# Kernel tuning notes

Measured on AMD Instinct MI355X. Metric: run time of the kernel, lower is better.

The kernel has to match this reference:

```python
import jax, jax.numpy as jnp
import numpy as np

B, L, D = 2, 2048, 2048
H, HKV, HD = 32, 8, 64
G = H // HKV  # GQA group size


def _rope(t, cos, sin):
    # t: [B, h, L, HD]; cos/sin: [L, HD//2]; pairs are consecutive (view_as_complex)
    tr, ti = t[..., 0::2], t[..., 1::2]
    out_r = tr * cos - ti * sin
    out_i = tr * sin + ti * cos
    return jnp.stack([out_r, out_i], axis=-1).reshape(t.shape)


def setup_inputs() -> dict:
    key = jax.random.key(0)
    ks = jax.random.split(key, 5)
    x = jax.random.normal(ks[0], (B, L, D), dtype=jnp.float32)
    wq = jax.random.normal(ks[1], (D, H * HD), dtype=jnp.float32) * 0.02
    wk = jax.random.normal(ks[2], (D, HKV * HD), dtype=jnp.float32) * 0.02
    wv = jax.random.normal(ks[3], (D, HKV * HD), dtype=jnp.float32) * 0.02
    wo = jax.random.normal(ks[4], (D, D), dtype=jnp.float32) * 0.02
    # RoPE freqs: theta_i = 10000^(-2i/HD), angle[p, i] = p * theta_i
    inv_freq = 1.0 / (10000.0 ** (jnp.arange(0, HD, 2, dtype=jnp.float32) / HD))
    angles = jnp.arange(L, dtype=jnp.float32)[:, None] * inv_freq[None, :]  # [L, HD//2]
    freqs_cos = jnp.cos(angles)
    freqs_sin = jnp.sin(angles)
    # additive causal mask [L, L]
    mask = jnp.where(jnp.tril(jnp.ones((L, L), dtype=bool)), 0.0, -1e9).astype(jnp.float32)
    return {"x": x, "wq": wq, "wk": wk, "wv": wv, "wo": wo,
            "freqs_cos": freqs_cos, "freqs_sin": freqs_sin, "mask": mask}


def reference(x, wq, wk, wv, wo, freqs_cos, freqs_sin, mask):
    b, l, _ = x.shape
    q = (x @ wq).reshape(b, l, H, HD).transpose(0, 2, 1, 3)      # [B, H, L, HD]
    k = (x @ wk).reshape(b, l, HKV, HD).transpose(0, 2, 1, 3)    # [B, HKV, L, HD]
    v = (x @ wv).reshape(b, l, HKV, HD).transpose(0, 2, 1, 3)
    q = _rope(q, freqs_cos, freqs_sin)
    k = _rope(k, freqs_cos, freqs_sin)
    # native GQA broadcast instead of repeat_kv copy (same math)
    qg = q.reshape(b, HKV, G, l, HD)
    scores = jnp.einsum("bhgqd,bhkd->bhgqk", qg, k) / jnp.sqrt(jnp.float32(HD))
    scores = scores + mask  # [B, HKV, G, L, L]
    probs = jax.nn.softmax(scores.astype(jnp.float32), axis=-1).astype(v.dtype)
    out = jnp.einsum("bhgqk,bhkd->bhgqd", probs, v)              # [B, HKV, G, L, HD]
    out = out.reshape(b, H, l, HD).transpose(0, 2, 1, 3).reshape(b, l, H * HD)
    return out @ wo
```

## Files before the change

### kernel.cpp

```cpp
#include <hip/hip_runtime.h>
#include <hip/hip_bf16.h>

#define B_   2
#define L_   2048
#define D_   2048
#define H_   32
#define HKV_ 8
#define HD_  64
#define G_   4
#define M_   4096
#define NF_  3072

typedef __attribute__((ext_vector_type(8))) short bf16x8;
typedef __attribute__((ext_vector_type(4))) float f32x4;

static __device__ __forceinline__ unsigned short f2bf(float f) {
  unsigned int u = __float_as_uint(f);
  unsigned int r = (u + 0x7FFFu + ((u >> 16) & 1u)) >> 16;
  return (unsigned short)r;
}
static __device__ __forceinline__ unsigned short f2bf_hw(float f) {
  __hip_bfloat16 h = __float2bfloat16(f);
  return *(unsigned short*)&h;
}

#define GLD16(g, l) __builtin_amdgcn_global_load_lds(                      \
    (const __attribute__((address_space(1))) void*)(g),                    \
    (__attribute__((address_space(3))) void*)(l), 16, 0, 0)

__global__ void cast_bf16_kernel(const float* __restrict__ in,
                                 unsigned short* __restrict__ out, int n4) {
  int i = blockIdx.x * blockDim.x + threadIdx.x;
  if (i >= n4) return;
  float4 v = ((const float4*)in)[i];
  uint2 r;
  r.x = (unsigned int)f2bf(v.x) | ((unsigned int)f2bf(v.y) << 16);
  r.y = (unsigned int)f2bf(v.z) | ((unsigned int)f2bf(v.w) << 16);
  ((uint2*)out)[i] = r;
}

__global__ void transpose_cast_kernel(const float* __restrict__ src,
                                      unsigned short* __restrict__ dst,
                                      int K, int N) {
  __shared__ float tile[32][33];
  int k0 = blockIdx.y * 32, n0 = blockIdx.x * 32;
  int tx = threadIdx.x, ty = threadIdx.y;
#pragma unroll
  for (int r = 0; r < 4; ++r)
    tile[ty * 4 + r][tx] = src[(size_t)(k0 + ty * 4 + r) * N + n0 + tx];
  __syncthreads();
#pragma unroll
  for (int r = 0; r < 4; ++r)
    dst[(size_t)(n0 + ty * 4 + r) * K + k0 + tx] = f2bf(tile[tx][ty * 4 + r]);
}

__global__ __launch_bounds__(256)
void gemm_bt_kernel(const unsigned short* __restrict__ A,
                    const unsigned short* __restrict__ Bt,
                    float* __restrict__ C, int M, int N, int K) {
  __shared__ unsigned short Al[128 * 32];
  __shared__ unsigned short Bl[128 * 32];
  const int tid = threadIdx.x;
  const int w = tid >> 6;
  const int l = tid & 63;
  const int row0 = blockIdx.y * 128;
  const int col0 = blockIdx.x * 128;
  const int wr = (w >> 1) * 64, wc = (w & 1) * 64;

  f32x4 acc[4][4];
#pragma unroll
  for (int m = 0; m < 4; ++m)
#pragma unroll
    for (int n = 0; n < 4; ++n) acc[m][n] = (f32x4){0.f, 0.f, 0.f, 0.f};

  const int srow = l >> 2;
  const int scol = (l & 3) * 8;
  const int fr = l & 15, fk = (l >> 4) * 8;
  const int nk = K / 32;

  for (int kt = 0; kt < nk; ++kt) {
    const int k0 = kt * 32;
#pragma unroll
    for (int t = 0; t < 2; ++t) {
      const int rr = (w * 2 + t) * 16 + srow;
      GLD16(A + (size_t)(row0 + rr) * K + k0 + scol, &Al[(w * 2 + t) * 512]);
      GLD16(Bt + (size_t)(col0 + rr) * K + k0 + scol, &Bl[(w * 2 + t) * 512]);
    }
    __syncthreads();
    bf16x8 af[4], bfr[4];
#pragma unroll
    for (int m = 0; m < 4; ++m)
      af[m] = *(const bf16x8*)&Al[(wr + m * 16 + fr) * 32 + fk];
#pragma unroll
    for (int n = 0; n < 4; ++n)
      bfr[n] = *(const bf16x8*)&Bl[(wc + n * 16 + fr) * 32 + fk];
#pragma unroll
    for (int m = 0; m < 4; ++m)
#pragma unroll
      for (int n = 0; n < 4; ++n)
        acc[m][n] = __builtin_amdgcn_mfma_f32_16x16x32_bf16(af[m], bfr[n], acc[m][n], 0, 0, 0);
    __syncthreads();
  }

  const int fq = l >> 4;
#pragma unroll
  for (int m = 0; m < 4; ++m)
#pragma unroll
    for (int n = 0; n < 4; ++n)
#pragma unroll
      for (int j = 0; j < 4; ++j) {
        int r = row0 + wr + m * 16 + fq * 4 + j;
        int c = col0 + wc + n * 16 + fr;
        C[(size_t)r * N + c] = acc[m][n][j];
      }
}

__global__ void rope_kernel(const float* __restrict__ src,
                            const float* __restrict__ cosf,
                            const float* __restrict__ sinf,
                            unsigned short* __restrict__ dst, int nh, int col_off,
                            float scale, int total) {
  int idx = blockIdx.x * blockDim.x + threadIdx.x;
  if (idx >= total) return;
  int g = idx & 7;
  int h = (idx >> 3) & (nh - 1);
  int row = idx / (nh << 3);
  int lpos = row & (L_ - 1);
  int b = row >> 11;
  const float* s = src + (size_t)row * NF_ + col_off + h * 64 + g * 8;
  float4 v0 = *(const float4*)s;
  float4 v1 = *(const float4*)(s + 4);
  float4 c4 = *(const float4*)(cosf + lpos * 32 + g * 4);
  float4 s4 = *(const float4*)(sinf + lpos * 32 + g * 4);
  float o0 = (v0.x * c4.x - v0.y * s4.x) * scale;
  float o1 = (v0.x * s4.x + v0.y * c4.x) * scale;
  float o2 = (v0.z * c4.y - v0.w * s4.y) * scale;
  float o3 = (v0.z * s4.y + v0.w * c4.y) * scale;
  float o4 = (v1.x * c4.z - v1.y * s4.z) * scale;
  float o5 = (v1.x * s4.z + v1.y * c4.z) * scale;
  float o6 = (v1.z * c4.w - v1.w * s4.w) * scale;
  float o7 = (v1.z * s4.w + v1.w * c4.w) * scale;
  uint4 r;
  r.x = (unsigned int)f2bf(o0) | ((unsigned int)f2bf(o1) << 16);
  r.y = (unsigned int)f2bf(o2) | ((unsigned int)f2bf(o3) << 16);
  r.z = (unsigned int)f2bf(o4) | ((unsigned int)f2bf(o5) << 16);
  r.w = (unsigned int)f2bf(o6) | ((unsigned int)f2bf(o7) << 16);
  *(uint4*)&dst[(((size_t)(b * nh + h)) * L_ + lpos) * 64 + g * 8] = r;
}

__global__ void cast_vT_kernel(const float* __restrict__ v,
                               unsigned short* __restrict__ vT) {
  __shared__ float tile[32][33];
  int l0 = blockIdx.x * 32, d0 = blockIdx.y * 32;
  int z = blockIdx.z;
  int b = z >> 3, hkv = z & 7;
  int tx = threadIdx.x, ty = threadIdx.y;
  const float* src = v + (size_t)(b * L_) * NF_ + 2560 + hkv * 64;
#pragma unroll
  for (int r = 0; r < 4; ++r)
    tile[ty * 4 + r][tx] = src[(size_t)(l0 + ty * 4 + r) * NF_ + d0 + tx];
  __syncthreads();
  unsigned short* dst = vT + ((size_t)z * 64) * L_;
#pragma unroll
  for (int r = 0; r < 4; ++r)
    dst[(size_t)(d0 + ty * 4 + r) * L_ + l0 + tx] = f2bf(tile[tx][ty * 4 + r]);
}

__global__ __launch_bounds__(256)
void attn_kernel(const unsigned short* __restrict__ Q,
                 const unsigned short* __restrict__ Kt,
                 const unsigned short* __restrict__ Vt,
                 unsigned short* __restrict__ O) {
  __shared__ unsigned short Kl[2][64 * 64];
  __shared__ unsigned short Vl[2][64 * 64];
  __shared__ unsigned short Pl[64 * 64];
  const int tid = threadIdx.x, w = tid >> 6, l = tid & 63;
  const int lin = blockIdx.y * 16 + blockIdx.x;
  const int work = ((lin & 7) << 7) + (lin >> 3);
  const int bh = work >> 4, by = work & 15;
  const int b = bh >> 5, h = bh & 31;
  const int hkv = h >> 2;
  const int q0 = by * 128;
  const int fr = l & 15, hi = l >> 4;
  const int frx = fr & 7;

  const int srow = l >> 3;
  const int scole = ((l & 7) ^ srow) * 8;

  const unsigned short* kbase = Kt + ((size_t)(b * HKV_ + hkv)) * L_ * 64;
  const unsigned short* vbase = Vt + ((size_t)(b * HKV_ + hkv)) * 64 * L_;

  bf16x8 qf[2][2];
#pragma unroll
  for (int s = 0; s < 2; ++s) {
    const unsigned short* qb =
        Q + (((size_t)bh) * L_ + q0 + s * 64 + w * 16 + fr) * 64 + hi * 8;
    qf[s][0] = *(const bf16x8*)(qb);
    qf[s][1] = *(const bf16x8*)(qb + 32);
  }

  float m_i[2][4], l_p[2][4];
  f32x4 oacc[2][4];
#pragma unroll
  for (int s = 0; s < 2; ++s)
#pragma unroll
    for (int j = 0; j < 4; ++j) { m_i[s][j] = -1e30f; l_p[s][j] = 0.f; }
#pragma unroll
  for (int s = 0; s < 2; ++s)
#pragma unroll
    for (int nf = 0; nf < 4; ++nf) oacc[s][nf] = (f32x4){0.f, 0.f, 0.f, 0.f};

  const int nt = 2 * by + 2;

#define ASTAGE(kv0_, buf_) do {                                              \
    _Pragma("unroll")                                                        \
    for (int u_ = 0; u_ < 2; ++u_) {                                         \
      const int c_ = w * 2 + u_;                                             \
      const int rr_ = c_ * 8 + srow;                                         \
      GLD16(kbase + ((size_t)((kv0_) + rr_)) * 64 + scole,                   \
            &Kl[buf_][c_ * 512]);                                            \
      GLD16(vbase + ((size_t)rr_) * L_ + (kv0_) + scole,                     \
            &Vl[buf_][c_ * 512]);                                            \
    }                                                                        \
  } while (0)

  ASTAGE(0, 0);

  for (int t = 0; t < nt; ++t) {
    const int buf = t & 1;
    if (t + 1 < nt) {
      ASTAGE((t + 1) * 64, buf ^ 1);
      asm volatile("s_waitcnt vmcnt(4)" ::: "memory");
    } else {
      asm volatile("s_waitcnt vmcnt(0)" ::: "memory");
    }
    __builtin_amdgcn_s_barrier();

    const int kv0 = t * 64;
#pragma unroll
    for (int s = 0; s < 2; ++s) {
      const int dlim = 2 * by + s;
      if (t > dlim) continue;

      f32x4 sacc[4];
#pragma unroll
      for (int nf = 0; nf < 4; ++nf) sacc[nf] = (f32x4){0.f, 0.f, 0.f, 0.f};
      __builtin_amdgcn_s_setprio(1);
#pragma unroll
      for (int ks = 0; ks < 2; ++ks) {
#pragma unroll
        for (int nf = 0; nf < 4; ++nf) {
          bf16x8 kfrag = *(const bf16x8*)
              &Kl[buf][(nf * 16 + fr) * 64 + (((ks * 4 + hi) ^ frx) * 8)];
          sacc[nf] = __builtin_amdgcn_mfma_f32_16x16x32_bf16(qf[s][ks], kfrag, sacc[nf], 0, 0, 0);
        }
      }
      __builtin_amdgcn_s_setprio(0);

      if (t == dlim) {
        const int rbase = q0 + s * 64 + w * 16 + hi * 4;
#pragma unroll
        for (int nf = 0; nf < 4; ++nf)
#pragma unroll
          for (int j = 0; j < 4; ++j)
            if (kv0 + nf * 16 + fr > rbase + j) sacc[nf][j] = -1e30f;
      }

      float rowmax[4];
#pragma unroll
      for (int j = 0; j < 4; ++j) {
        float mx = fmaxf(fmaxf(sacc[0][j], sacc[1][j]),
                         fmaxf(sacc[2][j], sacc[3][j]));
        mx = fmaxf(mx, __shfl_xor(mx, 1));
        mx = fmaxf(mx, __shfl_xor(mx, 2));
        mx = fmaxf(mx, __shfl_xor(mx, 4));
        mx = fmaxf(mx, __shfl_xor(mx, 8));
        rowmax[j] = mx;
      }

      float g = rowmax[0] - m_i[s][0];
      g = fmaxf(g, rowmax[1] - m_i[s][1]);
      g = fmaxf(g, rowmax[2] - m_i[s][2]);
      g = fmaxf(g, rowmax[3] - m_i[s][3]);
      if (!__all(g <= 8.f)) {
#pragma unroll
        for (int j = 0; j < 4; ++j) {
          float mnew = fmaxf(m_i[s][j], rowmax[j]);
          float cr = exp2f(m_i[s][j] - mnew);
          m_i[s][j] = mnew;
          l_p[s][j] *= cr;
#pragma unroll
          for (int nf = 0; nf < 4; ++nf) oacc[s][nf][j] *= cr;
        }
      }

#pragma unroll
      for (int j = 0; j < 4; ++j) {
        const int prow = w * 16 + hi * 4 + j;
#pragma unroll
        for (int nf = 0; nf < 4; ++nf) {
          float p = exp2f(sacc[nf][j] - m_i[s][j]);
          l_p[s][j] += p;
          Pl[prow * 64 + (((nf * 2 + (fr >> 3)) ^ (prow & 7)) * 8) + frx] =
              f2bf_hw(p);
        }
      }

      __builtin_amdgcn_s_setprio(1);
#pragma unroll
      for (int ks = 0; ks < 2; ++ks) {
        bf16x8 pa = *(const bf16x8*)
            &Pl[(w * 16 + fr) * 64 + (((ks * 4 + hi) ^ frx) * 8)];
#pragma unroll
        for (int nf = 0; nf < 4; ++nf) {
          bf16x8 vfrag = *(const bf16x8*)
              &Vl[buf][(nf * 16 + fr) * 64 + (((ks * 4 + hi) ^ frx) * 8)];
          oacc[s][nf] = __builtin_amdgcn_mfma_f32_16x16x32_bf16(pa, vfrag, oacc[s][nf], 0, 0, 0);
        }
      }
      __builtin_amdgcn_s_setprio(0);
    }
    __builtin_amdgcn_s_barrier();
  }
#undef ASTAGE

#pragma unroll
  for (int s = 0; s < 2; ++s)
#pragma unroll
    for (int j = 0; j < 4; ++j) {
      float lsum = l_p[s][j];
      lsum += __shfl_xor(lsum, 1);
      lsum += __shfl_xor(lsum, 2);
      lsum += __shfl_xor(lsum, 4);
      lsum += __shfl_xor(lsum, 8);
      float inv = 1.0f / lsum;
#pragma unroll
      for (int nf = 0; nf < 4; ++nf) {
        int qrow = q0 + s * 64 + w * 16 + hi * 4 + j;
        int d = nf * 16 + fr;
        O[((size_t)(b * L_ + qrow)) * 2048 + h * 64 + d] =
            f2bf_hw(oacc[s][nf][j] * inv);
      }
    }
}

extern "C" void kernel_launch(void* const* d_in, const int* in_sizes, int n_in,
                              void* d_out, int out_size, void* d_ws, size_t ws_size,
                              hipStream_t stream) {
  (void)in_sizes; (void)n_in; (void)out_size; (void)ws_size;
  const float* x  = (const float*)d_in[0];
  const float* wq = (const float*)d_in[1];
  const float* wk = (const float*)d_in[2];
  const float* wv = (const float*)d_in[3];
  const float* wo = (const float*)d_in[4];
  const float* fc = (const float*)d_in[5];
  const float* fs = (const float*)d_in[6];
  float* out = (float*)d_out;

  char* ws = (char*)d_ws;
  unsigned short* x_b  = (unsigned short*)(ws + 0);
  unsigned short* wT   = (unsigned short*)(ws + 16777216);
  unsigned short* woT  = (unsigned short*)(ws + 29360128);
  float* qkv_f         = (float*)(ws + 37748736);
  unsigned short* at_b = (unsigned short*)(ws + 37748736);
  unsigned short* q_b  = (unsigned short*)(ws + 88080384);
  unsigned short* k_b  = (unsigned short*)(ws + 104857600);
  unsigned short* vT_b = (unsigned short*)(ws + 109051904);

  const float qscale = 0.125f * 1.4426950408889634f;

  dim3 tb(32, 8);
  cast_bf16_kernel<<<8192, 256, 0, stream>>>(x, x_b, M_ * D_ / 4);
  transpose_cast_kernel<<<dim3(64, 64), tb, 0, stream>>>(wq, wT, 2048, 2048);
  transpose_cast_kernel<<<dim3(16, 64), tb, 0, stream>>>(wk, wT + (size_t)2048 * 2048, 2048, 512);
  transpose_cast_kernel<<<dim3(16, 64), tb, 0, stream>>>(wv, wT + (size_t)2560 * 2048, 2048, 512);
  transpose_cast_kernel<<<dim3(64, 64), tb, 0, stream>>>(wo, woT, 2048, 2048);

  gemm_bt_kernel<<<dim3(24, 32), 256, 0, stream>>>(x_b, wT, qkv_f, M_, NF_, 2048);

  rope_kernel<<<4096, 256, 0, stream>>>(qkv_f, fc, fs, q_b, 32, 0, qscale, M_ * 32 * 8);
  rope_kernel<<<1024, 256, 0, stream>>>(qkv_f, fc, fs, k_b, 8, 2048, 1.0f, M_ * 8 * 8);
  cast_vT_kernel<<<dim3(64, 2, 16), tb, 0, stream>>>(qkv_f, vT_b);

  attn_kernel<<<dim3(16, 64), 256, 0, stream>>>(q_b, k_b, vT_b, at_b);

  gemm_bt_kernel<<<dim3(16, 32), 256, 0, stream>>>(at_b, woT, out, M_, 2048, 2048);
}
```

Measured before the change: 449.4 us.

## Balance causal attention by pairing opposite query tiles per block

Each attention block now processes two 64-row query tiles, p and 31-p, in sequence, so every block runs exactly 33 KV tile iterations instead of a count that grows with its query position. This removes the load imbalance of causal attention, where late-row blocks did far more work and set the tail. The per-iteration loop now runs one tile's compute instead of two, so K/V staging is no longer shared across both query halves and the KV prefetch address logic becomes more complex. Separately, the three Q/K/V weight transpose-casts are merged into one launch to save launch overhead.

```diff
diff --git a/kernel.cpp b/kernel.cpp
--- a/kernel.cpp
+++ b/kernel.cpp
@@ -52,6 +52,27 @@
 #pragma unroll
   for (int r = 0; r < 4; ++r)
     dst[(size_t)(n0 + ty * 4 + r) * K + k0 + tx] = f2bf(tile[tx][ty * 4 + r]);
+}
+
+__global__ void transpose_cast_qkv_kernel(const float* __restrict__ wq,
+                                          const float* __restrict__ wk,
+                                          const float* __restrict__ wv,
+                                          unsigned short* __restrict__ dst) {
+  __shared__ float tile[32][33];
+  int n0 = blockIdx.x * 32, k0 = blockIdx.y * 32;
+  const float* src;
+  int ns, N;
+  if (n0 < 2048)      { src = wq; ns = n0;        N = 2048; }
+  else if (n0 < 2560) { src = wk; ns = n0 - 2048; N = 512; }
+  else                { src = wv; ns = n0 - 2560; N = 512; }
+  int tx = threadIdx.x, ty = threadIdx.y;
+#pragma unroll
+  for (int r = 0; r < 4; ++r)
+    tile[ty * 4 + r][tx] = src[(size_t)(k0 + ty * 4 + r) * N + ns + tx];
+  __syncthreads();
+#pragma unroll
+  for (int r = 0; r < 4; ++r)
+    dst[(size_t)(n0 + ty * 4 + r) * 2048 + k0 + tx] = f2bf(tile[tx][ty * 4 + r]);
 }
 
 __global__ __launch_bounds__(256)
@@ -177,10 +198,11 @@
   const int tid = threadIdx.x, w = tid >> 6, l = tid & 63;
   const int lin = blockIdx.y * 16 + blockIdx.x;
   const int work = ((lin & 7) << 7) + (lin >> 3);
-  const int bh = work >> 4, by = work & 15;
+  const int bh = work >> 4, p = work & 15;
   const int b = bh >> 5, h = bh & 31;
   const int hkv = h >> 2;
-  const int q0 = by * 128;
+  const int byA = p, byB = 31 - p;
+  const int q0A = byA * 64, q0B = byB * 64;
   const int fr = l & 15, hi = l >> 4;
   const int frx = fr & 7;
 
@@ -193,8 +215,9 @@
   bf16x8 qf[2][2];
 #pragma unroll
   for (int s = 0; s < 2; ++s) {
+    const int qq0 = s ? q0B : q0A;
     const unsigned short* qb =
-        Q + (((size_t)bh) * L_ + q0 + s * 64 + w * 16 + fr) * 64 + hi * 8;
+        Q + (((size_t)bh) * L_ + qq0 + w * 16 + fr) * 64 + hi * 8;
     qf[s][0] = *(const bf16x8*)(qb);
     qf[s][1] = *(const bf16x8*)(qb + 32);
   }
@@ -209,8 +232,6 @@
   for (int s = 0; s < 2; ++s)
 #pragma unroll
     for (int nf = 0; nf < 4; ++nf) oacc[s][nf] = (f32x4){0.f, 0.f, 0.f, 0.f};
-
-  const int nt = 2 * by + 2;
 
 #define ASTAGE(kv0_, buf_) do {                                              \
     _Pragma("unroll")                                                        \
@@ -224,108 +245,112 @@
     }                                                                        \
   } while (0)
 
+#define COMPUTE(H_) do {                                                     \
+    const int qq0 = (H_) ? q0B : q0A;                                        \
+    f32x4 sacc[4];                                                           \
+    _Pragma("unroll")                                                        \
+    for (int nf = 0; nf < 4; ++nf) sacc[nf] = (f32x4){0.f, 0.f, 0.f, 0.f};   \
+    __builtin_amdgcn_s_setprio(1);                                           \
+    _Pragma("unroll")                                                        \
+    for (int ks = 0; ks < 2; ++ks) {                                         \
+      _Pragma("unroll")                                                      \
+      for (int nf = 0; nf < 4; ++nf) {                                       \
+        bf16x8 kfrag = *(const bf16x8*)                                      \
+            &Kl[buf][(nf * 16 + fr) * 64 + (((ks * 4 + hi) ^ frx) * 8)];     \
+        sacc[nf] = __builtin_amdgcn_mfma_f32_16x16x32_bf16(                  \
+            qf[H_][ks], kfrag, sacc[nf], 0, 0, 0);                           \
+      }                                                                      \
+    }                                                                        \
+    __builtin_amdgcn_s_setprio(0);                                           \
+    if (diag) {                                                              \
+      const int rbase = qq0 + w * 16 + hi * 4;                               \
+      _Pragma("unroll")                                                      \
+      for (int nf = 0; nf < 4; ++nf)                                         \
+        _Pragma("unroll")                                                    \
+        for (int j = 0; j < 4; ++j)                                          \
+          if (kv0 + nf * 16 + fr > rbase + j) sacc[nf][j] = -1e30f;          \
+    }                                                                        \
+    float rowmax[4];                                                         \
+    _Pragma("unroll")                                                        \
+    for (int j = 0; j < 4; ++j) {                                            \
+      float mx = fmaxf(fmaxf(sacc[0][j], sacc[1][j]),                        \
+                       fmaxf(sacc[2][j], sacc[3][j]));                       \
+      mx = fmaxf(mx, __shfl_xor(mx, 1));                                     \
+      mx = fmaxf(mx, __shfl_xor(mx, 2));                                     \
+      mx = fmaxf(mx, __shfl_xor(mx, 4));                                     \
+      mx = fmaxf(mx, __shfl_xor(mx, 8));                                     \
+      rowmax[j] = mx;                                                        \
+    }                                                                        \
+    float g = rowmax[0] - m_i[H_][0];                                        \
+    g = fmaxf(g, rowmax[1] - m_i[H_][1]);                                    \
+    g = fmaxf(g, rowmax[2] - m_i[H_][2]);                                    \
+    g = fmaxf(g, rowmax[3] - m_i[H_][3]);                                    \
+    if (!__all(g <= 8.f)) {                                                  \
+      _Pragma("unroll")                                                      \
+      for (int j = 0; j < 4; ++j) {                                          \
+        float mnew = fmaxf(m_i[H_][j], rowmax[j]);                           \
+        float cr = exp2f(m_i[H_][j] - mnew);                                 \
+        m_i[H_][j] = mnew;                                                   \
+        l_p[H_][j] *= cr;                                                    \
+        _Pragma("unroll")                                                    \
+        for (int nf = 0; nf < 4; ++nf) oacc[H_][nf][j] *= cr;                \
+      }                                                                      \
+    }                                                                        \
+    _Pragma("unroll")                                                        \
+    for (int j = 0; j < 4; ++j) {                                            \
+      const int prow = w * 16 + hi * 4 + j;                                  \
+      _Pragma("unroll")                                                      \
+      for (int nf = 0; nf < 4; ++nf) {                                       \
+        float pv = exp2f(sacc[nf][j] - m_i[H_][j]);                          \
+        l_p[H_][j] += pv;                                                    \
+        Pl[prow * 64 + (((nf * 2 + (fr >> 3)) ^ (prow & 7)) * 8) + frx] =    \
+            f2bf_hw(pv);                                                     \
+      }                                                                      \
+    }                                                                        \
+    __builtin_amdgcn_s_setprio(1);                                           \
+    _Pragma("unroll")                                                        \
+    for (int ks = 0; ks < 2; ++ks) {                                         \
+      bf16x8 pa = *(const bf16x8*)                                           \
+          &Pl[(w * 16 + fr) * 64 + (((ks * 4 + hi) ^ frx) * 8)];             \
+      _Pragma("unroll")                                                      \
+      for (int nf = 0; nf < 4; ++nf) {                                       \
+        bf16x8 vfrag = *(const bf16x8*)                                      \
+            &Vl[buf][(nf * 16 + fr) * 64 + (((ks * 4 + hi) ^ frx) * 8)];     \
+        oacc[H_][nf] = __builtin_amdgcn_mfma_f32_16x16x32_bf16(              \
+            pa, vfrag, oacc[H_][nf], 0, 0, 0);                               \
+      }                                                                      \
+    }                                                                        \
+    __builtin_amdgcn_s_setprio(0);                                           \
+  } while (0)
+
   ASTAGE(0, 0);
 
-  for (int t = 0; t < nt; ++t) {
-    const int buf = t & 1;
-    if (t + 1 < nt) {
-      ASTAGE((t + 1) * 64, buf ^ 1);
+  for (int job = 0; job <= 32; ++job) {
+    const int buf = job & 1;
+    const int half = (job > byA) ? 1 : 0;
+    const int kv0 = (half ? (job - byA - 1) : job) * 64;
+    const bool diag = (job == byA) || (job == 32);
+
+    if (job < 32) {
+      const int nxt_half = ((job + 1) > byA) ? 1 : 0;
+      const int nxt_kv0 = (nxt_half ? (job - byA) : (job + 1)) * 64;
+      ASTAGE(nxt_kv0, buf ^ 1);
       asm volatile("s_waitcnt vmcnt(4)" ::: "memory");
     } else {
       asm volatile("s_waitcnt vmcnt(0)" ::: "memory");
     }
     __builtin_amdgcn_s_barrier();
 
-    const int kv0 = t * 64;
-#pragma unroll
-    for (int s = 0; s < 2; ++s) {
-      const int dlim = 2 * by + s;
-      if (t > dlim) continue;
-
-      f32x4 sacc[4];
-#pragma unroll
-      for (int nf = 0; nf < 4; ++nf) sacc[nf] = (f32x4){0.f, 0.f, 0.f, 0.f};
-      __builtin_amdgcn_s_setprio(1);
-#pragma unroll
-      for (int ks = 0; ks < 2; ++ks) {
-#pragma unroll
-        for (int nf = 0; nf < 4; ++nf) {
-          bf16x8 kfrag = *(const bf16x8*)
-              &Kl[buf][(nf * 16 + fr) * 64 + (((ks * 4 + hi) ^ frx) * 8)];
-          sacc[nf] = __builtin_amdgcn_mfma_f32_16x16x32_bf16(qf[s][ks], kfrag, sacc[nf], 0, 0, 0);
-        }
-      }
-      __builtin_amdgcn_s_setprio(0);
-
-      if (t == dlim) {
-        const int rbase = q0 + s * 64 + w * 16 + hi * 4;
-#pragma unroll
-        for (int nf = 0; nf < 4; ++nf)
-#pragma unroll
-          for (int j = 0; j < 4; ++j)
-            if (kv0 + nf * 16 + fr > rbase + j) sacc[nf][j] = -1e30f;
-      }
-
-      float rowmax[4];
-#pragma unroll
-      for (int j = 0; j < 4; ++j) {
-        float mx = fmaxf(fmaxf(sacc[0][j], sacc[1][j]),
-                         fmaxf(sacc[2][j], sacc[3][j]));
-        mx = fmaxf(mx, __shfl_xor(mx, 1));
-        mx = fmaxf(mx, __shfl_xor(mx, 2));
-        mx = fmaxf(mx, __shfl_xor(mx, 4));
-        mx = fmaxf(mx, __shfl_xor(mx, 8));
-        rowmax[j] = mx;
-      }
-
-      float g = rowmax[0] - m_i[s][0];
-      g = fmaxf(g, rowmax[1] - m_i[s][1]);
-      g = fmaxf(g, rowmax[2] - m_i[s][2]);
-      g = fmaxf(g, rowmax[3] - m_i[s][3]);
-      if (!__all(g <= 8.f)) {
-#pragma unroll
-        for (int j = 0; j < 4; ++j) {
-          float mnew = fmaxf(m_i[s][j], rowmax[j]);
-          float cr = exp2f(m_i[s][j] - mnew);
-          m_i[s][j] = mnew;
-          l_p[s][j] *= cr;
-#pragma unroll
-          for (int nf = 0; nf < 4; ++nf) oacc[s][nf][j] *= cr;
-        }
-      }
-
-#pragma unroll
-      for (int j = 0; j < 4; ++j) {
-        const int prow = w * 16 + hi * 4 + j;
-#pragma unroll
-        for (int nf = 0; nf < 4; ++nf) {
-          float p = exp2f(sacc[nf][j] - m_i[s][j]);
-          l_p[s][j] += p;
-          Pl[prow * 64 + (((nf * 2 + (fr >> 3)) ^ (prow & 7)) * 8) + frx] =
-              f2bf_hw(p);
-        }
-      }
-
-      __builtin_amdgcn_s_setprio(1);
-#pragma unroll
-      for (int ks = 0; ks < 2; ++ks) {
-        bf16x8 pa = *(const bf16x8*)
-            &Pl[(w * 16 + fr) * 64 + (((ks * 4 + hi) ^ frx) * 8)];
-#pragma unroll
-        for (int nf = 0; nf < 4; ++nf) {
-          bf16x8 vfrag = *(const bf16x8*)
-              &Vl[buf][(nf * 16 + fr) * 64 + (((ks * 4 + hi) ^ frx) * 8)];
-          oacc[s][nf] = __builtin_amdgcn_mfma_f32_16x16x32_bf16(pa, vfrag, oacc[s][nf], 0, 0, 0);
-        }
-      }
-      __builtin_amdgcn_s_setprio(0);
-    }
+    if (half == 0) COMPUTE(0); else COMPUTE(1);
+
     __builtin_amdgcn_s_barrier();
   }
 #undef ASTAGE
-
-#pragma unroll
-  for (int s = 0; s < 2; ++s)
+#undef COMPUTE
+
+#pragma unroll
+  for (int s = 0; s < 2; ++s) {
+    const int qq0 = s ? q0B : q0A;
 #pragma unroll
     for (int j = 0; j < 4; ++j) {
       float lsum = l_p[s][j];
@@ -336,12 +361,13 @@
       float inv = 1.0f / lsum;
 #pragma unroll
       for (int nf = 0; nf < 4; ++nf) {
-        int qrow = q0 + s * 64 + w * 16 + hi * 4 + j;
+        int qrow = qq0 + w * 16 + hi * 4 + j;
         int d = nf * 16 + fr;
         O[((size_t)(b * L_ + qrow)) * 2048 + h * 64 + d] =
             f2bf_hw(oacc[s][nf][j] * inv);
       }
     }
+  }
 }
 
 extern "C" void kernel_launch(void* const* d_in, const int* in_sizes, int n_in,
@@ -371,9 +397,7 @@
 
   dim3 tb(32, 8);
   cast_bf16_kernel<<<8192, 256, 0, stream>>>(x, x_b, M_ * D_ / 4);
-  transpose_cast_kernel<<<dim3(64, 64), tb, 0, stream>>>(wq, wT, 2048, 2048);
-  transpose_cast_kernel<<<dim3(16, 64), tb, 0, stream>>>(wk, wT + (size_t)2048 * 2048, 2048, 512);
-  transpose_cast_kernel<<<dim3(16, 64), tb, 0, stream>>>(wv, wT + (size_t)2560 * 2048, 2048, 512);
+  transpose_cast_qkv_kernel<<<dim3(96, 64), tb, 0, stream>>>(wq, wk, wv, wT);
   transpose_cast_kernel<<<dim3(64, 64), tb, 0, stream>>>(wo, woT, 2048, 2048);
 
   gemm_bt_kernel<<<dim3(24, 32), 256, 0, stream>>>(x_b, wT, qkv_f, M_, NF_, 2048);
```

Result: faster. 403.4 us (-10.2%).
